# Kernel optimization log

Measured on AMD Instinct MI355X. Metric: run time of the kernel, lower is better.

The kernel has to match this reference:

```python
import jax, jax.numpy as jnp
import numpy as np

ROPE_BASE = 1000000.0
EPS = 1e-6
N_HEADS = 16

def apply_rope(x, base=ROPE_BASE):
    # x: [b, seq, heads, head_dim]
    b, seq, n_heads, dim = x.shape
    half = dim // 2
    i = jnp.arange(half)
    theta = 1.0 / base ** (2 * i / dim)
    pos = jnp.arange(seq)
    angles = pos[:, None] * theta[None, :]            # [seq, half]
    cos = jnp.cos(angles)[None, :, None, :]
    sin = jnp.sin(angles)[None, :, None, :]
    x1, x2 = jnp.split(x, 2, axis=-1)
    return jnp.concatenate([x1 * cos - x2 * sin, x1 * sin + x2 * cos], axis=-1)

def setup_inputs() -> dict:
    key = jax.random.key(0)
    ks = jax.random.split(key, 6)
    b, seq, dim = 2, 2048, 1024
    scale = 1.0 / np.sqrt(dim)
    return {
        "x": jax.random.normal(ks[0], (b, seq, dim), dtype=jnp.float32),
        "norm_scale": jnp.ones((dim,), dtype=jnp.float32),
        "Wq": jax.random.normal(ks[1], (dim, dim), dtype=jnp.float32) * scale,
        "Wk": jax.random.normal(ks[2], (dim, dim), dtype=jnp.float32) * scale,
        "Wv": jax.random.normal(ks[3], (dim, dim), dtype=jnp.float32) * scale,
        "Wo": jax.random.normal(ks[4], (dim, dim), dtype=jnp.float32) * scale,
    }

def reference(x, norm_scale, Wq, Wk, Wv, Wo):
    b, seq, d = x.shape
    n_heads = N_HEADS
    dh = d // n_heads
    # RMSNorm
    var = jnp.mean(jnp.square(x), axis=-1, keepdims=True)
    x_norm = x * jax.lax.rsqrt(var + EPS) * norm_scale
    # QKV projections ([in,out] weights as in nnx.Linear)
    q = (x_norm @ Wq).reshape(b, seq, n_heads, dh)
    k = (x_norm @ Wk).reshape(b, seq, n_heads, dh)
    v = (x_norm @ Wv).reshape(b, seq, n_heads, dh)
    q = apply_rope(q)
    k = apply_rope(k)
    # causal attention with explicit score matrix (faithful to source)
    scores = jnp.einsum('bthd,bshd->bhts', q, k) / jnp.sqrt(jnp.float32(dh))
    causal = jnp.triu(jnp.full((seq, seq), -jnp.inf, dtype=jnp.float32), k=1)
    scores = scores + causal[None, None, :, :]
    weights = jax.nn.softmax(scores, axis=-1)
    out = jnp.einsum('bhts,bshd->bthd', weights, v).reshape(b, seq, d)
    return out @ Wo
```

## Files before the change

### kernel.cpp

```cpp
#include <hip/hip_runtime.h>

typedef unsigned short ushort_t;
typedef __attribute__((ext_vector_type(8))) short short8;
typedef __attribute__((ext_vector_type(4))) short short4v;
typedef __attribute__((ext_vector_type(4))) float floatx4;

#define DEV static __device__ __forceinline__
#define NEG_BIG (-1e30f)

typedef const __attribute__((address_space(1))) unsigned int* gas_ptr;
typedef __attribute__((address_space(3))) unsigned int* las_ptr;

DEV void async16(const ushort_t* g, ushort_t* l) {
    __builtin_amdgcn_global_load_lds((gas_ptr)(const void*)g, (las_ptr)(void*)l, 16, 0, 0);
}

DEV float bf2f(ushort_t u) {
    union { unsigned u; float f; } v; v.u = ((unsigned)u) << 16; return v.f;
}
DEV ushort_t f2bf(float f) {
    union { float f; unsigned u; } v; v.f = f;
    unsigned r = v.u + 0x7FFF + ((v.u >> 16) & 1);
    return (ushort_t)(r >> 16);
}
DEV ushort_t f2bf_trunc(float f) {
    union { float f; unsigned u; } v; v.f = f;
    return (ushort_t)(v.u >> 16);
}
DEV float load_bf16_scrub(const ushort_t* p, size_t i) {
    ushort_t u = p[i];
    if (((u >> 7) & 0xFF) == 0xFF) u = 0;
    return bf2f(u);
}
DEV float load_f32_scrub(const ushort_t* p, size_t i) {
    unsigned u = ((const unsigned*)p)[i];
    if (((u >> 23) & 0xFF) == 0xFF) u = 0;
    union { unsigned u; float f; } v; v.u = u; return v.f;
}

DEV int probe_is_f32(const ushort_t* __restrict__ p) {
    int tid = threadIdx.x + threadIdx.y * blockDim.x;
    int nthr = blockDim.x * blockDim.y;
    __shared__ int cnt;
    if (tid == 0) cnt = 0;
    __syncthreads();
    int weird = 0;
    for (int i = tid; i < 2048; i += nthr) {
        unsigned e = (p[i] >> 7) & 0xFF;
        weird += (e >= 0x90) ? 1 : 0;
    }
#pragma unroll
    for (int off = 32; off; off >>= 1) weird += __shfl_xor(weird, off);
    if ((tid & 63) == 0) atomicAdd(&cnt, weird);
    __syncthreads();
    return cnt > 16;
}

__global__ void prep_kernel(const ushort_t* __restrict__ W0,
                            const ushort_t* __restrict__ W1,
                            const ushort_t* __restrict__ W2,
                            const ushort_t* __restrict__ W3,
                            ushort_t* __restrict__ WTq3,
                            ushort_t* __restrict__ WoT,
                            const ushort_t* __restrict__ x,
                            const ushort_t* __restrict__ g,
                            ushort_t* __restrict__ xn) {
    int is_f32 = probe_is_f32(x);
    int z = blockIdx.z;
    if (z < 4) {
        const ushort_t* W = (z == 0) ? W0 : (z == 1) ? W1 : (z == 2) ? W2 : W3;
        __shared__ ushort_t tile[32][33];
        int tx = threadIdx.x, ty = threadIdx.y;
        int xx = blockIdx.x * 32 + tx;
        int y0 = blockIdx.y * 32;
#pragma unroll
        for (int j = 0; j < 32; j += 8) {
            size_t idx = (size_t)(y0 + ty + j) * 1024 + xx;
            tile[ty + j][tx] = f2bf(is_f32 ? load_f32_scrub(W, idx) : load_bf16_scrub(W, idx));
        }
        __syncthreads();
        int nx = blockIdx.y * 32 + tx;
        ushort_t* dst = (z < 3) ? WTq3 : WoT;
        int ny0 = blockIdx.x * 32 + ((z < 3) ? z * 1024 : 0);
#pragma unroll
        for (int j = 0; j < 32; j += 8)
            dst[(size_t)(ny0 + ty + j) * 1024 + nx] = tile[tx][ty + j];
    } else {
        int row = (z - 4) * 1024 + blockIdx.y * 32 + blockIdx.x;
        int tid = threadIdx.y * 32 + threadIdx.x;
        float vals[4], gv[4];
        size_t base = (size_t)row * 1024 + tid * 4;
#pragma unroll
        for (int i = 0; i < 4; i++) {
            if (is_f32) {
                vals[i] = load_f32_scrub(x, base + i);
                gv[i]   = load_f32_scrub(g, tid * 4 + i);
            } else {
                vals[i] = load_bf16_scrub(x, base + i);
                gv[i]   = load_bf16_scrub(g, tid * 4 + i);
            }
        }
        float ss = vals[0]*vals[0] + vals[1]*vals[1] + vals[2]*vals[2] + vals[3]*vals[3];
#pragma unroll
        for (int off = 32; off > 0; off >>= 1) ss += __shfl_xor(ss, off);
        __shared__ float red[4];
        if ((tid & 63) == 0) red[tid >> 6] = ss;
        __syncthreads();
        ss = red[0] + red[1] + red[2] + red[3];
        float inv = rsqrtf(ss * (1.0f / 1024.0f) + 1e-6f);
#pragma unroll
        for (int i = 0; i < 4; i++)
            xn[base + i] = f2bf(vals[i] * inv * gv[i]);
    }
}

__global__ __launch_bounds__(256, 4) void gemm_qkv(const ushort_t* __restrict__ A,
                                                   const ushort_t* __restrict__ Bt,
                                                   ushort_t* __restrict__ qb,
                                                   ushort_t* __restrict__ kb,
                                                   ushort_t* __restrict__ vt) {
    const int K = 1024;
    int tid = threadIdx.x;
    int lane = tid & 63, w = tid >> 6;
    int c = lane & 15, quad = lane >> 4;
    int mh = w >> 1, nh = w & 1;
    int lin = blockIdx.y * gridDim.x + blockIdx.x;
    int xcd = lin & 7, idx = lin >> 3;
    int bm = ((xcd & 3) * 8 + (idx & 7)) * 128;
    int bn = ((xcd >> 2) * 12 + (idx >> 3)) * 128;
    int lr = lane >> 2, lq = lane & 3;

    __shared__ __align__(16) ushort_t As[16 * 512];
    __shared__ __align__(16) ushort_t Bs[16 * 512];

    const floatx4 zero = {0.f, 0.f, 0.f, 0.f};
    floatx4 acc[4][4];
#pragma unroll
    for (int i = 0; i < 4; i++)
#pragma unroll
        for (int j = 0; j < 4; j++) acc[i][j] = zero;

    for (int k0 = 0; k0 < K; k0 += 64) {
        __syncthreads();
#pragma unroll
        for (int ci = 0; ci < 8; ci++) {
            int ch = w * 8 + ci;
            if (ch < 16) {
                int rg = ch >> 1, kc = ch & 1;
                async16(A + (size_t)(bm + rg * 16 + lr) * K + k0 + kc * 32 + lq * 8,
                        As + ch * 512);
            } else {
                int b2 = ch - 16;
                int rg = b2 >> 1, kc = b2 & 1;
                async16(Bt + (size_t)(bn + rg * 16 + lr) * K + k0 + kc * 32 + lq * 8,
                        Bs + b2 * 512);
            }
        }
        __syncthreads();
#pragma unroll
        for (int kc = 0; kc < 2; kc++) {
            short8 af[4], bf[4];
#pragma unroll
            for (int i = 0; i < 4; i++)
                af[i] = *(const short8*)(As + ((mh * 4 + i) * 2 + kc) * 512 + c * 32 + quad * 8);
#pragma unroll
            for (int j = 0; j < 4; j++)
                bf[j] = *(const short8*)(Bs + ((nh * 4 + j) * 2 + kc) * 512 + c * 32 + quad * 8);
#pragma unroll
            for (int i = 0; i < 4; i++)
#pragma unroll
                for (int j = 0; j < 4; j++)
                    acc[i][j] = __builtin_amdgcn_mfma_f32_16x16x32_bf16(af[i], bf[j], acc[i][j], 0, 0, 0);
        }
    }

    int proj = bn >> 10;
    int n0 = (bn & 1023) + nh * 64;
    if (proj < 2) {
        float th0 = exp2f((float)c * (-19.931568569324174f / 32.0f));
        float th1 = exp2f((float)(16 + c) * (-19.931568569324174f / 32.0f));
        float scale = (proj == 0) ? 0.125f : 1.0f;
#pragma unroll
        for (int i = 0; i < 4; i++)
#pragma unroll
            for (int r = 0; r < 4; r++) {
                int s = (bm + mh * 64 + i * 16 + quad * 4 + r) & 2047;
                float a0 = (float)s * th0, a1 = (float)s * th1;
                float sn0 = __sinf(a0), cs0 = __cosf(a0);
                float sn1 = __sinf(a1), cs1 = __cosf(a1);
                float x1a = acc[i][0][r], x2a = acc[i][2][r];
                acc[i][0][r] = (x1a * cs0 - x2a * sn0) * scale;
                acc[i][2][r] = (x1a * sn0 + x2a * cs0) * scale;
                float x1b = acc[i][1][r], x2b = acc[i][3][r];
                acc[i][1][r] = (x1b * cs1 - x2b * sn1) * scale;
                acc[i][3][r] = (x1b * sn1 + x2b * cs1) * scale;
            }
        ushort_t* dst = (proj == 0) ? qb : kb;
#pragma unroll
        for (int i = 0; i < 4; i++)
#pragma unroll
            for (int j = 0; j < 4; j++)
#pragma unroll
                for (int r = 0; r < 4; r++) {
                    int row = bm + mh * 64 + i * 16 + quad * 4 + r;
                    dst[(size_t)row * 1024 + n0 + j * 16 + c] = f2bf(acc[i][j][r]);
                }
    } else {
#pragma unroll
        for (int i = 0; i < 4; i++) {
            int row0 = bm + mh * 64 + i * 16 + quad * 4;
            int b = row0 >> 11, s0v = row0 & 2047;
#pragma unroll
            for (int j = 0; j < 4; j++) {
                int col = n0 + j * 16 + c;
                int hh = col >> 6, dh = col & 63;
                short4v pk;
#pragma unroll
                for (int r = 0; r < 4; r++) pk[r] = (short)f2bf(acc[i][j][r]);
                *(short4v*)(vt + (size_t)((b * 16 + hh) * 64 + dh) * 2048 + s0v) = pk;
            }
        }
    }
}

__global__ __launch_bounds__(256, 4) void gemm_out(const ushort_t* __restrict__ A,
                                                   const ushort_t* __restrict__ Bt,
                                                   float* __restrict__ C) {
    const int K = 1024, N = 1024;
    int tid = threadIdx.x;
    int lane = tid & 63, w = tid >> 6;
    int c = lane & 15, quad = lane >> 4;
    int mh = w >> 1, nh = w & 1;
    int lin = blockIdx.y * gridDim.x + blockIdx.x;
    int xcd = lin & 7, idx = lin >> 3;
    int bm = ((xcd & 3) * 8 + (idx & 7)) * 128;
    int bn = ((xcd >> 2) * 8 + (idx >> 3)) * 64;
    int lr = lane >> 2, lq = lane & 3;

    __shared__ __align__(16) ushort_t As[16 * 512];
    __shared__ __align__(16) ushort_t Bs[8 * 512];

    const floatx4 zero = {0.f, 0.f, 0.f, 0.f};
    floatx4 acc[4][2];
#pragma unroll
    for (int i = 0; i < 4; i++)
#pragma unroll
        for (int j = 0; j < 2; j++) acc[i][j] = zero;

    for (int k0 = 0; k0 < K; k0 += 64) {
        __syncthreads();
#pragma unroll
        for (int ci = 0; ci < 6; ci++) {
            int ch = w * 6 + ci;
            if (ch < 16) {
                int rg = ch >> 1, kc = ch & 1;
                async16(A + (size_t)(bm + rg * 16 + lr) * K + k0 + kc * 32 + lq * 8,
                        As + ch * 512);
            } else {
                int b2 = ch - 16;
                int rg = b2 >> 1, kc = b2 & 1;
                async16(Bt + (size_t)(bn + rg * 16 + lr) * K + k0 + kc * 32 + lq * 8,
                        Bs + b2 * 512);
            }
        }
        __syncthreads();
#pragma unroll
        for (int kc = 0; kc < 2; kc++) {
            short8 af[4], bf[2];
#pragma unroll
            for (int i = 0; i < 4; i++)
                af[i] = *(const short8*)(As + ((mh * 4 + i) * 2 + kc) * 512 + c * 32 + quad * 8);
#pragma unroll
            for (int j = 0; j < 2; j++)
                bf[j] = *(const short8*)(Bs + ((nh * 2 + j) * 2 + kc) * 512 + c * 32 + quad * 8);
#pragma unroll
            for (int i = 0; i < 4; i++)
#pragma unroll
                for (int j = 0; j < 2; j++)
                    acc[i][j] = __builtin_amdgcn_mfma_f32_16x16x32_bf16(af[i], bf[j], acc[i][j], 0, 0, 0);
        }
    }
#pragma unroll
    for (int i = 0; i < 4; i++)
#pragma unroll
        for (int j = 0; j < 2; j++)
#pragma unroll
            for (int r = 0; r < 4; r++) {
                int row = bm + mh * 64 + i * 16 + quad * 4 + r;
                int col = bn + nh * 32 + j * 16 + c;
                C[(size_t)row * N + col] = acc[i][j][r];
            }
}

__global__ __launch_bounds__(256) void attn_kernel(const ushort_t* __restrict__ q,
                                                   const ushort_t* __restrict__ k,
                                                   const ushort_t* __restrict__ vt,
                                                   ushort_t* __restrict__ o) {
    int tid = threadIdx.x;
    int lane = tid & 63, w = tid >> 6;
    int c = lane & 15, quad = lane >> 4;
    int bh = blockIdx.x;
    int b = bh >> 4, h = bh & 15;
    int qt = 31 - (int)blockIdx.y;
    int lr = lane >> 2, lq = lane & 3;
    const ushort_t* qb  = q + (size_t)b * 2048 * 1024 + h * 64;
    const ushort_t* kbp = k + (size_t)b * 2048 * 1024 + h * 64;
    const ushort_t* vtb = vt + (size_t)(b * 16 + h) * 64 * 2048;
    ushort_t* ob = o + (size_t)b * 2048 * 1024 + h * 64;

    __shared__ __align__(16) ushort_t Ks[2][8 * 512];
    __shared__ __align__(16) ushort_t Vs[2][8 * 512];
    __shared__ __align__(16) ushort_t Ps[64 * 72];

    const floatx4 zero = {0.f, 0.f, 0.f, 0.f};

    int t0b = qt * 64;
    int t0w = t0b + w * 16;
    int ntile = qt + 1;

    const ushort_t* qrow = qb + (size_t)(t0w + c) * 1024;
    short8 aq0 = *(const short8*)(qrow + quad * 8);
    short8 aq1 = *(const short8*)(qrow + 32 + quad * 8);

    float l_part[4];
    floatx4 oacc[4];
#pragma unroll
    for (int r = 0; r < 4; r++) l_part[r] = 0.f;
#pragma unroll
    for (int dt = 0; dt < 4; dt++) oacc[dt] = zero;

#pragma unroll
    for (int ci = 0; ci < 4; ci++) {
        int ch = w * 4 + ci;
        if (ch < 8) {
            int nt = ch >> 1, hf = ch & 1;
            async16(kbp + (size_t)(nt * 16 + lr) * 1024 + hf * 32 + lq * 8,
                    Ks[0] + ch * 512);
        } else {
            int dt = (ch - 8) >> 1, hf = ch & 1;
            async16(vtb + (size_t)(dt * 16 + lr) * 2048 + hf * 32 + lq * 8,
                    Vs[0] + (ch - 8) * 512);
        }
    }

    for (int kt = 0; kt < ntile; kt++) {
        __syncthreads();
        int cur = kt & 1;
        if (kt + 1 < ntile) {
            int s1 = (kt + 1) * 64;
            int nxt = cur ^ 1;
#pragma unroll
            for (int ci = 0; ci < 4; ci++) {
                int ch = w * 4 + ci;
                if (ch < 8) {
                    int nt = ch >> 1, hf = ch & 1;
                    async16(kbp + (size_t)(s1 + nt * 16 + lr) * 1024 + hf * 32 + lq * 8,
                            Ks[nxt] + ch * 512);
                } else {
                    int dt = (ch - 8) >> 1, hf = ch & 1;
                    async16(vtb + (size_t)(dt * 16 + lr) * 2048 + s1 + hf * 32 + lq * 8,
                            Vs[nxt] + (ch - 8) * 512);
                }
            }
        }
        int s0 = kt * 64;

        floatx4 sacc[4];
#pragma unroll
        for (int nt = 0; nt < 4; nt++) sacc[nt] = zero;
#pragma unroll
        for (int nt = 0; nt < 4; nt++) {
            short8 b0 = *(const short8*)(Ks[cur] + nt * 1024 + c * 32 + quad * 8);
            short8 b1 = *(const short8*)(Ks[cur] + nt * 1024 + 512 + c * 32 + quad * 8);
            sacc[nt] = __builtin_amdgcn_mfma_f32_16x16x32_bf16(aq0, b0, sacc[nt], 0, 0, 0);
            sacc[nt] = __builtin_amdgcn_mfma_f32_16x16x32_bf16(aq1, b1, sacc[nt], 0, 0, 0);
        }

        if (kt == ntile - 1) {
#pragma unroll
            for (int r = 0; r < 4; r++) {
                int t = t0w + quad * 4 + r;
                float ps = 0.f;
#pragma unroll
                for (int nt = 0; nt < 4; nt++) {
                    float v = (s0 + nt * 16 + c > t) ? NEG_BIG : sacc[nt][r];
                    float e = __expf(v);
                    ps += e;
                    Ps[(w * 16 + quad * 4 + r) * 72 + nt * 16 + c] = f2bf_trunc(e);
                }
                l_part[r] += ps;
            }
        } else {
#pragma unroll
            for (int r = 0; r < 4; r++) {
                float ps = 0.f;
#pragma unroll
                for (int nt = 0; nt < 4; nt++) {
                    float e = __expf(sacc[nt][r]);
                    ps += e;
                    Ps[(w * 16 + quad * 4 + r) * 72 + nt * 16 + c] = f2bf_trunc(e);
                }
                l_part[r] += ps;
            }
        }

        short8 pa0 = *(const short8*)(Ps + (w * 16 + c) * 72 + quad * 8);
        short8 pa1 = *(const short8*)(Ps + (w * 16 + c) * 72 + 32 + quad * 8);
#pragma unroll
        for (int dt = 0; dt < 4; dt++) {
            short8 v0 = *(const short8*)(Vs[cur] + dt * 1024 + c * 32 + quad * 8);
            short8 v1 = *(const short8*)(Vs[cur] + dt * 1024 + 512 + c * 32 + quad * 8);
            oacc[dt] = __builtin_amdgcn_mfma_f32_16x16x32_bf16(pa0, v0, oacc[dt], 0, 0, 0);
            oacc[dt] = __builtin_amdgcn_mfma_f32_16x16x32_bf16(pa1, v1, oacc[dt], 0, 0, 0);
        }
    }

    float linv[4];
#pragma unroll
    for (int r = 0; r < 4; r++) {
        float l = l_part[r];
#pragma unroll
        for (int off = 1; off < 16; off <<= 1) l += __shfl_xor(l, off);
        linv[r] = 1.0f / l;
    }
#pragma unroll
    for (int dt = 0; dt < 4; dt++)
#pragma unroll
        for (int r = 0; r < 4; r++) {
            int t = t0w + quad * 4 + r;
            ob[(size_t)t * 1024 + dt * 16 + c] = f2bf_trunc(oacc[dt][r] * linv[r]);
        }
}

extern "C" void kernel_launch(void* const* d_in, const int* in_sizes, int n_in,
                              void* d_out, int out_size, void* d_ws, size_t ws_size,
                              hipStream_t stream) {
    const ushort_t* x  = (const ushort_t*)d_in[0];
    const ushort_t* g  = (const ushort_t*)d_in[1];
    const ushort_t* Wq = (const ushort_t*)d_in[2];
    const ushort_t* Wk = (const ushort_t*)d_in[3];
    const ushort_t* Wv = (const ushort_t*)d_in[4];
    const ushort_t* Wo = (const ushort_t*)d_in[5];

    char* ws = (char*)d_ws;
    const size_t MB = 1ull << 20;
    ushort_t* xn   = (ushort_t*)(ws);
    ushort_t* qb   = (ushort_t*)(ws + 8 * MB);
    ushort_t* kb   = (ushort_t*)(ws + 16 * MB);
    ushort_t* vt   = (ushort_t*)(ws + 24 * MB);
    ushort_t* WTq3 = (ushort_t*)(ws + 32 * MB);
    ushort_t* WoT  = (ushort_t*)(ws + 38 * MB);
    ushort_t* at   = xn;

    prep_kernel<<<dim3(32, 32, 8), dim3(32, 8), 0, stream>>>(Wq, Wk, Wv, Wo, WTq3, WoT, x, g, xn);

    gemm_qkv<<<dim3(24, 32), 256, 0, stream>>>(xn, WTq3, qb, kb, vt);

    attn_kernel<<<dim3(32, 32), 256, 0, stream>>>(qb, kb, vt, at);

    gemm_out<<<dim3(16, 32), 256, 0, stream>>>(at, WoT, (float*)d_out);
}
```

Before: 185.5 us.

## Keep softmax probabilities in registers via transposed QK^T and swizzled V tiles

Swaps the operands of the QK^T MFMA so each lane holds a key-column slice of the score tile, which can feed the P·V MFMA directly as 16x16x16 bf16 A-operands. This removes the Ps shared-memory round trip and the per-row 16-lane reductions. The V tile loads are swizzled to match, and the row sum now uses fewer shuffles. It also adds s_setprio around the MFMA blocks and a launch-bounds occupancy hint of 5, at the cost of twice as many P·V MFMA instructions, each of smaller K.

```diff
diff --git a/kernel.cpp b/kernel.cpp
--- a/kernel.cpp
+++ b/kernel.cpp
@@ -7,6 +7,8 @@
 
 #define DEV static __device__ __forceinline__
 #define NEG_BIG (-1e30f)
+
+#define MFMA16(a, b, c) __builtin_amdgcn_mfma_f32_16x16x16bf16_1k((a), (b), (c), 0, 0, 0)
 
 typedef const __attribute__((address_space(1))) unsigned int* gas_ptr;
 typedef __attribute__((address_space(3))) unsigned int* las_ptr;
@@ -292,10 +294,10 @@
             }
 }
 
-__global__ __launch_bounds__(256) void attn_kernel(const ushort_t* __restrict__ q,
-                                                   const ushort_t* __restrict__ k,
-                                                   const ushort_t* __restrict__ vt,
-                                                   ushort_t* __restrict__ o) {
+__global__ __launch_bounds__(256, 5) void attn_kernel(const ushort_t* __restrict__ q,
+                                                      const ushort_t* __restrict__ k,
+                                                      const ushort_t* __restrict__ vt,
+                                                      ushort_t* __restrict__ o) {
     int tid = threadIdx.x;
     int lane = tid & 63, w = tid >> 6;
     int c = lane & 15, quad = lane >> 4;
@@ -303,6 +305,7 @@
     int b = bh >> 4, h = bh & 15;
     int qt = 31 - (int)blockIdx.y;
     int lr = lane >> 2, lq = lane & 3;
+    int vb = (lq - lr) & 3;
     const ushort_t* qb  = q + (size_t)b * 2048 * 1024 + h * 64;
     const ushort_t* kbp = k + (size_t)b * 2048 * 1024 + h * 64;
     const ushort_t* vtb = vt + (size_t)(b * 16 + h) * 64 * 2048;
@@ -310,7 +313,6 @@
 
     __shared__ __align__(16) ushort_t Ks[2][8 * 512];
     __shared__ __align__(16) ushort_t Vs[2][8 * 512];
-    __shared__ __align__(16) ushort_t Ps[64 * 72];
 
     const floatx4 zero = {0.f, 0.f, 0.f, 0.f};
 
@@ -322,10 +324,11 @@
     short8 aq0 = *(const short8*)(qrow + quad * 8);
     short8 aq1 = *(const short8*)(qrow + 32 + quad * 8);
 
-    float l_part[4];
+    int voffA = c * 32 + (((quad >> 1) + c) & 3) * 8 + (quad & 1) * 4;
+    int voffB = c * 32 + (((quad >> 1) + 2 + c) & 3) * 8 + (quad & 1) * 4;
+
+    float l_sum = 0.f;
     floatx4 oacc[4];
-#pragma unroll
-    for (int r = 0; r < 4; r++) l_part[r] = 0.f;
 #pragma unroll
     for (int dt = 0; dt < 4; dt++) oacc[dt] = zero;
 
@@ -338,7 +341,7 @@
                     Ks[0] + ch * 512);
         } else {
             int dt = (ch - 8) >> 1, hf = ch & 1;
-            async16(vtb + (size_t)(dt * 16 + lr) * 2048 + hf * 32 + lq * 8,
+            async16(vtb + (size_t)(dt * 16 + lr) * 2048 + hf * 32 + vb * 8,
                     Vs[0] + (ch - 8) * 512);
         }
     }
@@ -358,7 +361,7 @@
                             Ks[nxt] + ch * 512);
                 } else {
                     int dt = (ch - 8) >> 1, hf = ch & 1;
-                    async16(vtb + (size_t)(dt * 16 + lr) * 2048 + s1 + hf * 32 + lq * 8,
+                    async16(vtb + (size_t)(dt * 16 + lr) * 2048 + s1 + hf * 32 + vb * 8,
                             Vs[nxt] + (ch - 8) * 512);
                 }
             }
@@ -368,61 +371,71 @@
         floatx4 sacc[4];
 #pragma unroll
         for (int nt = 0; nt < 4; nt++) sacc[nt] = zero;
+        __builtin_amdgcn_s_setprio(1);
 #pragma unroll
         for (int nt = 0; nt < 4; nt++) {
-            short8 b0 = *(const short8*)(Ks[cur] + nt * 1024 + c * 32 + quad * 8);
-            short8 b1 = *(const short8*)(Ks[cur] + nt * 1024 + 512 + c * 32 + quad * 8);
-            sacc[nt] = __builtin_amdgcn_mfma_f32_16x16x32_bf16(aq0, b0, sacc[nt], 0, 0, 0);
-            sacc[nt] = __builtin_amdgcn_mfma_f32_16x16x32_bf16(aq1, b1, sacc[nt], 0, 0, 0);
-        }
-
+            short8 k0f = *(const short8*)(Ks[cur] + nt * 1024 + c * 32 + quad * 8);
+            short8 k1f = *(const short8*)(Ks[cur] + nt * 1024 + 512 + c * 32 + quad * 8);
+            sacc[nt] = __builtin_amdgcn_mfma_f32_16x16x32_bf16(k0f, aq0, sacc[nt], 0, 0, 0);
+            sacc[nt] = __builtin_amdgcn_mfma_f32_16x16x32_bf16(k1f, aq1, sacc[nt], 0, 0, 0);
+        }
+        __builtin_amdgcn_s_setprio(0);
+
+        short4v pa[4];
+        float ps = 0.f;
         if (kt == ntile - 1) {
-#pragma unroll
-            for (int r = 0; r < 4; r++) {
-                int t = t0w + quad * 4 + r;
-                float ps = 0.f;
-#pragma unroll
-                for (int nt = 0; nt < 4; nt++) {
-                    float v = (s0 + nt * 16 + c > t) ? NEG_BIG : sacc[nt][r];
-                    float e = __expf(v);
-                    ps += e;
-                    Ps[(w * 16 + quad * 4 + r) * 72 + nt * 16 + c] = f2bf_trunc(e);
+            int t = t0w + c;
+#pragma unroll
+            for (int nt = 0; nt < 4; nt++) {
+                float pn = 0.f;
+#pragma unroll
+                for (int r = 0; r < 4; r++) {
+                    int s = s0 + nt * 16 + quad * 4 + r;
+                    float e = __expf((s > t) ? NEG_BIG : sacc[nt][r]);
+                    pn += e;
+                    pa[nt][r] = (short)f2bf_trunc(e);
                 }
-                l_part[r] += ps;
+                ps += pn;
             }
         } else {
 #pragma unroll
-            for (int r = 0; r < 4; r++) {
-                float ps = 0.f;
-#pragma unroll
-                for (int nt = 0; nt < 4; nt++) {
+            for (int nt = 0; nt < 4; nt++) {
+                float pn = 0.f;
+#pragma unroll
+                for (int r = 0; r < 4; r++) {
                     float e = __expf(sacc[nt][r]);
-                    ps += e;
-                    Ps[(w * 16 + quad * 4 + r) * 72 + nt * 16 + c] = f2bf_trunc(e);
+                    pn += e;
+                    pa[nt][r] = (short)f2bf_trunc(e);
                 }
-                l_part[r] += ps;
-            }
-        }
-
-        short8 pa0 = *(const short8*)(Ps + (w * 16 + c) * 72 + quad * 8);
-        short8 pa1 = *(const short8*)(Ps + (w * 16 + c) * 72 + 32 + quad * 8);
+                ps += pn;
+            }
+        }
+        l_sum += ps;
+
+        __builtin_amdgcn_s_setprio(1);
 #pragma unroll
         for (int dt = 0; dt < 4; dt++) {
-            short8 v0 = *(const short8*)(Vs[cur] + dt * 1024 + c * 32 + quad * 8);
-            short8 v1 = *(const short8*)(Vs[cur] + dt * 1024 + 512 + c * 32 + quad * 8);
-            oacc[dt] = __builtin_amdgcn_mfma_f32_16x16x32_bf16(pa0, v0, oacc[dt], 0, 0, 0);
-            oacc[dt] = __builtin_amdgcn_mfma_f32_16x16x32_bf16(pa1, v1, oacc[dt], 0, 0, 0);
-        }
-    }
-
+            const ushort_t* vbase = Vs[cur] + dt * 1024;
+            short4v bv0 = *(const short4v*)(vbase + voffA);
+            short4v bv1 = *(const short4v*)(vbase + voffB);
+            short4v bv2 = *(const short4v*)(vbase + 512 + voffA);
+            short4v bv3 = *(const short4v*)(vbase + 512 + voffB);
+            oacc[dt] = MFMA16(pa[0], bv0, oacc[dt]);
+            oacc[dt] = MFMA16(pa[1], bv1, oacc[dt]);
+            oacc[dt] = MFMA16(pa[2], bv2, oacc[dt]);
+            oacc[dt] = MFMA16(pa[3], bv3, oacc[dt]);
+        }
+        __builtin_amdgcn_s_setprio(0);
+    }
+
+    float l = l_sum;
+    l += __shfl_xor(l, 16);
+    l += __shfl_xor(l, 32);
+    float linv0 = 1.0f / l;
     float linv[4];
 #pragma unroll
-    for (int r = 0; r < 4; r++) {
-        float l = l_part[r];
-#pragma unroll
-        for (int off = 1; off < 16; off <<= 1) l += __shfl_xor(l, off);
-        linv[r] = 1.0f / l;
-    }
+    for (int r = 0; r < 4; r++) linv[r] = __shfl(linv0, quad * 4 + r);
+
 #pragma unroll
     for (int dt = 0; dt < 4; dt++)
 #pragma unroll
```

New measurement: 206.3 us. 11.2% more time.
